# Optimization experiments

Hardware: AMD Instinct MI355X
Metric: run time of the kernel (lower is better)

Reference implementation:

```python
import jax, jax.numpy as jnp
import numpy as np


def setup_inputs() -> dict:
    key = jax.random.key(0)
    k1, k2, k3 = jax.random.split(key, 3)
    B, N, D = 64, 1024, 768
    inputs = jax.random.normal(k1, (B, N, D), dtype=jnp.float32)
    x_class = jax.random.normal(k2, (D,), dtype=jnp.float32)
    embeddings = jax.random.normal(k3, (N + 1, D), dtype=jnp.float32)
    return {"inputs": inputs, "x_class": x_class, "embeddings": embeddings}


def reference(inputs, x_class, embeddings):
    # The original tf.while_loop just broadcasts x_class over the batch dim.
    B = inputs.shape[0]
    cls = jnp.broadcast_to(x_class[None, None, :], (B, 1, inputs.shape[2]))  # [B,1,D]
    return jnp.concatenate([cls, inputs], axis=1) + embeddings  # [B,N+1,D]
```

## Files before the change

### kernel.cpp

```cpp
#include <hip/hip_runtime.h>
#include <hip/hip_bf16.h>


typedef float f4 __attribute__((ext_vector_type(4)));

#define D4      192
#define ROWS4   196800
#define BULK4   196608
#define BLKS    48
#define STRIDE  (BLKS * 256)
#define ITERS   16

__global__ __launch_bounds__(256)
void pos_embed_kernel(const f4* __restrict__ in4,
                      const f4* __restrict__ cls4,
                      const f4* __restrict__ emb4,
                      f4* __restrict__ out4) {
    const int b = blockIdx.y;
    const f4* __restrict__ inb  = in4  + (size_t)b * BULK4;
    f4* __restrict__       outb = out4 + (size_t)b * ROWS4;

    if (blockIdx.x == BLKS) {
        const int t = threadIdx.x;
        if (t < D4) {
            outb[t] = cls4[t] + emb4[t];
        }
        return;
    }

    int i = blockIdx.x * 256 + threadIdx.x;
    #pragma unroll
    for (int k = 0; k < ITERS; ++k, i += STRIDE) {
        f4 s = __builtin_nontemporal_load(&inb[i]);
        f4 e = emb4[D4 + i];
        f4 r = s + e;
        __builtin_nontemporal_store(r, &outb[D4 + i]);
    }
}

extern "C" void kernel_launch(void* const* d_in, const int* in_sizes, int n_in,
                              void* d_out, int out_size, void* d_ws, size_t ws_size,
                              hipStream_t stream) {
    const f4* in4  = (const f4*)d_in[0];
    const f4* cls4 = (const f4*)d_in[1];
    const f4* emb4 = (const f4*)d_in[2];
    f4* out4       = (f4*)d_out;

    dim3 grid(BLKS + 1, 64, 1);
    dim3 block(256, 1, 1);
    pos_embed_kernel<<<grid, block, 0, stream>>>(in4, cls4, emb4, out4);
}
```

Baseline: 330.2 us.

## Flatten grid and give each block a contiguous chunk with software-pipelined loads

Replaces the 2D grid of strided blocks with a 1D grid in which each block handles a contiguous 6144-vector chunk of one batch. Loads for the next step are issued before the current results are stored, a manual double-buffering scheme. The change also adds an occupancy hint to launch_bounds. The aim is better memory-level parallelism and locality for this bandwidth-bound add. The kernel is still limited by HBM bandwidth, so the gain may be small.

```diff
diff --git a/kernel.cpp b/kernel.cpp
--- a/kernel.cpp
+++ b/kernel.cpp
@@ -1,40 +1,62 @@
 #include <hip/hip_runtime.h>
-#include <hip/hip_bf16.h>
 
 
 typedef float f4 __attribute__((ext_vector_type(4)));
 
-#define D4      192
-#define ROWS4   196800
-#define BULK4   196608
-#define BLKS    48
-#define STRIDE  (BLKS * 256)
-#define ITERS   16
+#define D4        192
+#define ROWS4     196800
+#define BULK4     196608
+#define NB        64
+#define BULK_BLKS 2048
+#define PER_BLK   6144
+#define STEPS     12
 
-__global__ __launch_bounds__(256)
+__global__ __launch_bounds__(256, 8)
 void pos_embed_kernel(const f4* __restrict__ in4,
                       const f4* __restrict__ cls4,
                       const f4* __restrict__ emb4,
                       f4* __restrict__ out4) {
-    const int b = blockIdx.y;
-    const f4* __restrict__ inb  = in4  + (size_t)b * BULK4;
-    f4* __restrict__       outb = out4 + (size_t)b * ROWS4;
+    const int x = blockIdx.x;
 
-    if (blockIdx.x == BLKS) {
+    if (x >= BULK_BLKS) {
+        const int b = x - BULK_BLKS;
         const int t = threadIdx.x;
         if (t < D4) {
-            outb[t] = cls4[t] + emb4[t];
+            out4[(size_t)b * ROWS4 + t] = cls4[t] + emb4[t];
         }
         return;
     }
 
-    int i = blockIdx.x * 256 + threadIdx.x;
-    #pragma unroll
-    for (int k = 0; k < ITERS; ++k, i += STRIDE) {
-        f4 s = __builtin_nontemporal_load(&inb[i]);
-        f4 e = emb4[D4 + i];
-        f4 r = s + e;
-        __builtin_nontemporal_store(r, &outb[D4 + i]);
+    const int b  = x >> 5;
+    const int c  = x & 31;
+    const int i0 = c * PER_BLK + threadIdx.x;
+
+    const f4* __restrict__ ip = in4  + (size_t)b * BULK4 + i0;
+    const f4* __restrict__ ep = emb4 + D4 + i0;
+    f4*       __restrict__ op = out4 + (size_t)b * ROWS4 + D4 + i0;
+
+    f4 a0 = __builtin_nontemporal_load(ip);
+    f4 a1 = __builtin_nontemporal_load(ip + 256);
+    f4 e0 = ep[0];
+    f4 e1 = ep[256];
+
+    for (int k = 0; k < STEPS - 1; ++k) {
+        const int cur = k * 512;
+        const int nxt = cur + 512;
+        f4 b0 = __builtin_nontemporal_load(ip + nxt);
+        f4 b1 = __builtin_nontemporal_load(ip + nxt + 256);
+        f4 f0 = ep[nxt];
+        f4 f1 = ep[nxt + 256];
+        f4 r0 = a0 + e0;
+        f4 r1 = a1 + e1;
+        __builtin_nontemporal_store(r0, op + cur);
+        __builtin_nontemporal_store(r1, op + cur + 256);
+        a0 = b0; a1 = b1; e0 = f0; e1 = f1;
+    }
+    {
+        const int cur = (STEPS - 1) * 512;
+        __builtin_nontemporal_store(a0 + e0, op + cur);
+        __builtin_nontemporal_store(a1 + e1, op + cur + 256);
     }
 }
 
@@ -46,7 +68,7 @@
     const f4* emb4 = (const f4*)d_in[2];
     f4* out4       = (f4*)d_out;
 
-    dim3 grid(BLKS + 1, 64, 1);
+    dim3 grid(BULK_BLKS + NB, 1, 1);
     dim3 block(256, 1, 1);
     pos_embed_kernel<<<grid, block, 0, stream>>>(in4, cls4, emb4, out4);
 }
```

Measured after the change: 327.8 us. No clear change (-0.7%).
